# Optimization experiments

Hardware: AMD Instinct MI355X
Metric: run time of the kernel (lower is better)

Reference implementation:

```python
import jax, jax.numpy as jnp
import numpy as np

B, M, H, E, V, U = 1024, 15, 256, 256, 30000, 1000


def setup_inputs() -> dict:
    key = jax.random.key(0)
    ks = jax.random.split(key, 24)
    s = 0.05  # weight init scale
    return {
        "input_ids": jax.random.randint(ks[0], (B, 1), 0, V),
        "input_embedding": jax.random.normal(ks[1], (B, 1, E), jnp.float32),
        "hidden": jax.random.normal(ks[2], (1, B, H), jnp.float32),
        "inter_output": jax.random.normal(ks[3], (B, M, H), jnp.float32),
        "user_list": jax.random.randint(ks[4], (B,), 0, U),
        # per-user parameter tables (torch ModuleLists of Linear); stored [in,out]
        "inter_W": jax.random.normal(ks[5], (U, H, H), jnp.float32) * s,
        "inter_b": jax.random.normal(ks[6], (U, H), jnp.float32) * s,
        "hidden_W": jax.random.normal(ks[7], (U, H, H), jnp.float32) * s,
        "hidden_b": jax.random.normal(ks[8], (U, H), jnp.float32) * s,
        "lt1_W": jax.random.normal(ks[9], (U, 2 * H, H), jnp.float32) * s,
        "lt1_b": jax.random.normal(ks[10], (U, H), jnp.float32) * s,
        "scale_W": jax.random.normal(ks[11], (U, H), jnp.float32) * s,
        "scale_b": jax.random.normal(ks[12], (U,), jnp.float32) * s,
        # GRU (1 layer), torch layout: W_ih [3H, 2E], W_hh [3H, H], gate order r,z,n
        "gru_Wih": jax.random.normal(ks[13], (3 * H, 2 * E), jnp.float32) * s,
        "gru_Whh": jax.random.normal(ks[14], (3 * H, H), jnp.float32) * s,
        "gru_bih": jax.random.normal(ks[15], (3 * H,), jnp.float32) * s,
        "gru_bhh": jax.random.normal(ks[16], (3 * H,), jnp.float32) * s,
        # output projection, stored [H, V]
        "lin_W": jax.random.normal(ks[17], (H, V), jnp.float32) * s,
        "lin_b": jax.random.normal(ks[18], (V,), jnp.float32) * s,
    }


def reference(input_ids, input_embedding, hidden, inter_output, user_list,
              inter_W, inter_b, hidden_W, hidden_b, lt1_W, lt1_b,
              scale_W, scale_b, gru_Wih, gru_Whh, gru_bih, gru_bhh,
              lin_W, lin_b):
    embedded_input = input_embedding  # dropout p=0 (eval)
    hidden_t = jnp.transpose(hidden, (1, 0, 2))  # [B,1,H]

    # per-user intra attention: gather user weights, batched GEMMs (replaces python loop)
    Wi = inter_W[user_list]                      # [B,H,H]
    inter_output_a = jnp.einsum('bmh,bho->bmo', inter_output, Wi) + inter_b[user_list][:, None, :]
    Wh = hidden_W[user_list]                     # [B,H,H]
    hidden_t_a = jnp.einsum('bih,bho->bio', hidden_t, Wh) + hidden_b[user_list][:, None, :]  # [B,1,H]
    cat = jnp.concatenate([jnp.broadcast_to(hidden_t_a, (hidden_t_a.shape[0], M, H)), inter_output_a], axis=2)  # [B,M,2H]
    result = jnp.tanh(jnp.einsum('bmk,bko->bmo', cat, lt1_W[user_list]) + lt1_b[user_list][:, None, :])  # [B,M,H]
    energies = jnp.einsum('bmh,bh->bm', result, scale_W[user_list]) + scale_b[user_list][:, None]  # [B,M]

    attn_weights = jax.nn.softmax(energies, axis=1)                      # [B,M]
    context = jnp.einsum('bm,bmh->bh', attn_weights, inter_output)[:, None, :]  # [B,1,H]

    gru_input = jnp.concatenate([embedded_input, context], axis=2)  # [B,1,2E]
    x = gru_input[:, 0, :]
    h = hidden[0]
    gi = x @ gru_Wih.T + gru_bih   # [B,3H]
    gh = h @ gru_Whh.T + gru_bhh
    gi_r, gi_z, gi_n = jnp.split(gi, 3, axis=1)
    gh_r, gh_z, gh_n = jnp.split(gh, 3, axis=1)
    r = jax.nn.sigmoid(gi_r + gh_r)
    z = jax.nn.sigmoid(gi_z + gh_z)
    n = jnp.tanh(gi_n + r * gh_n)
    h_new = (1.0 - z) * n + z * h
    gru_output = h_new[:, None, :]       # [B,1,H]
    hidden_new = h_new[None, :, :]       # [1,B,H]

    output = gru_output @ lin_W + lin_b  # [B,1,V]
    return (output, hidden_new, embedded_input, gru_output, attn_weights)
```

## Files before the change

kernel.cpp:

```cpp
#include <hip/hip_runtime.h>
#include <math.h>

#define B 1024
#define M 15
#define H 256
#define E 256
#define V 30000
#define U 1000

typedef float  vf4    __attribute__((ext_vector_type(4)));
typedef __bf16 bf16x8 __attribute__((ext_vector_type(8)));
typedef float  f32x4  __attribute__((ext_vector_type(4)));

#define O_OUT   0
#define O_HID   ((size_t)B*V)
#define O_EMB   (O_HID + (size_t)B*H)
#define O_GRU   (O_EMB + (size_t)B*E)
#define O_ATT   (O_GRU + (size_t)B*H)

#define GLDS(g, l) __builtin_amdgcn_global_load_lds( \
    (const __attribute__((address_space(1))) void*)(g), \
    (__attribute__((address_space(3))) void*)(l), 16, 0, 0)

union BF8 { __bf16 h[8]; bf16x8 v; };
union BF4 { __bf16 h[4]; unsigned long long u; };

__global__ __launch_bounds__(1024) void sort_kernel(
    const int* __restrict__ ul, int* __restrict__ order, int* __restrict__ rbase_g)
{
    __shared__ int cnt[1024];
    __shared__ int base[1024];
    const int tid = threadIdx.x;
    cnt[tid] = 0;
    __syncthreads();
    const int u = ul[tid];
    atomicAdd(&cnt[u], 1);
    __syncthreads();
    int c0 = cnt[tid];
    int v  = c0;
    for (int off = 1; off < 1024; off <<= 1) {
        int add = (tid >= off) ? cnt[tid - off] : 0;
        __syncthreads();
        v += add;
        cnt[tid] = v;
        __syncthreads();
    }
    base[tid]   = v - c0;
    rbase_g[tid] = v - c0;
    __syncthreads();
    int pos = atomicAdd(&base[u], 1);
    order[pos] = tid;
}

#define FB_ATTN 1024
#define FB_TR   500
#define FB_WC   256
#define FB_TOT  (FB_ATTN + FB_TR + FB_WC)

__global__ __launch_bounds__(256, 3) void fused_pre_kernel(
    const float* __restrict__ hidden,
    const float* __restrict__ inter_output,
    const int*   __restrict__ user_list,
    const int*   __restrict__ order,
    const int*   __restrict__ rbase,
    const float* __restrict__ inter_W,
    const float* __restrict__ inter_b,
    const float* __restrict__ hidden_W,
    const float* __restrict__ hidden_b,
    const float* __restrict__ lt1_W,
    const float* __restrict__ lt1_b,
    const float* __restrict__ scale_W,
    const float* __restrict__ scale_b,
    const float* __restrict__ emb,
    const float* __restrict__ Wih,
    const float* __restrict__ Whh,
    const float* __restrict__ lin_W,
    float* __restrict__ out,
    __bf16* __restrict__ xcat,
    __bf16* __restrict__ wcat,
    __bf16* __restrict__ WT)
{
    __shared__ __align__(16) char smem[34432];
    const int bid = blockIdx.x;
    const int tid = threadIdx.x;

    if (bid >= FB_ATTN + FB_TR) {
        const int wb   = bid - (FB_ATTN + FB_TR);
        const int wave = tid >> 6, lane = tid & 63;
        const int n    = wb * 4 + wave;
        const int r    = (n >> 2) + ((n & 3) << 8);
        #pragma unroll
        for (int i = 0; i < 3; ++i) {
            int k = i * 256 + lane * 4;
            vf4 v = {0.f, 0.f, 0.f, 0.f};
            if (r < 512) {
                v = (k < 512) ? *(const vf4*)&Wih[(size_t)r * 512 + k]
                              : *(const vf4*)&Whh[(size_t)r * 256 + (k - 512)];
            } else if (r < 768) {
                if (k < 512) v = *(const vf4*)&Wih[(size_t)r * 512 + k];
            } else {
                if (k >= 512) v = *(const vf4*)&Whh[(size_t)(r - 256) * 256 + (k - 512)];
            }
            BF4 p;
            p.h[0]=(__bf16)v[0]; p.h[1]=(__bf16)v[1]; p.h[2]=(__bf16)v[2]; p.h[3]=(__bf16)v[3];
            *(unsigned long long*)&wcat[(size_t)n * 768 + k] = p.u;
        }
        return;
    }

    if (bid >= FB_ATTN) {
        const int t   = bid - FB_ATTN;
        const int v0  = (t % 125) * 240;
        const int k0  = (t / 125) * 64;
        const int lane = tid & 63, kq = tid >> 6;
        __bf16* T = (__bf16*)smem;

        if (lane < 60) {
            #pragma unroll
            for (int i = 0; i < 4; ++i) {
                int kr = kq * 16 + i * 4;
                vf4 f0 = *(const vf4*)&lin_W[(size_t)(k0 + kr + 0) * V + v0 + lane * 4];
                vf4 f1 = *(const vf4*)&lin_W[(size_t)(k0 + kr + 1) * V + v0 + lane * 4];
                vf4 f2 = *(const vf4*)&lin_W[(size_t)(k0 + kr + 2) * V + v0 + lane * 4];
                vf4 f3 = *(const vf4*)&lin_W[(size_t)(k0 + kr + 3) * V + v0 + lane * 4];
                #pragma unroll
                for (int j = 0; j < 4; ++j) {
                    BF4 pk;
                    pk.h[0] = (__bf16)f0[j];
                    pk.h[1] = (__bf16)f1[j];
                    pk.h[2] = (__bf16)f2[j];
                    pk.h[3] = (__bf16)f3[j];
                    int v = lane * 4 + j;
                    *(unsigned long long*)&T[v * 68 + kr] = pk.u;
                }
            }
        }
        __syncthreads();
        for (int r = 0; r < 15; ++r) {
            int L = r * 256 + tid;
            int v = L >> 4, c = L & 15;
            __builtin_nontemporal_store(
                *(const unsigned long long*)&T[v * 68 + c * 4],
                (unsigned long long*)&WT[(size_t)(v0 + v) * H + k0 + c * 4]);
        }
        return;
    }

    const int s   = ((bid & 7) << 7) + (bid >> 3);
    const int b0  = order[s];
    const int u   = user_list[b0];

    {
        float ev = emb[(size_t)b0 * E + tid];
        float hv = hidden[(size_t)b0 * H + tid];
        xcat[(size_t)b0 * 768 + tid]       = (__bf16)ev;
        xcat[(size_t)b0 * 768 + 512 + tid] = (__bf16)hv;
        __builtin_nontemporal_store(ev, &out[O_EMB + (size_t)b0 * E + tid]);
    }

    if ((s - rbase[u]) & 1) return;
    bool paired = false;
    int  b1 = b0;
    if (s + 1 < B) {
        int ob = order[s + 1];
        if (user_list[ob] == u) { paired = true; b1 = ob; }
    }

    const int lane = tid & 63;
    const int wave = tid >> 6;
    const int wn0  = wave * 64;

    __bf16* Abuf = (__bf16*)smem;
    __bf16* hta  = (__bf16*)(smem + 32768);
    float*  red  = (float*)(smem + 32768 + 1024);
    float*  e_lds= (float*)(smem + 32768 + 1024 + 512);

    {
        const int r    = tid >> 3;
        const int part = tid & 7;
        const int sm   = r >> 4;
        const int mr   = r & 15;
        const int bs   = sm ? b1 : b0;
        const bool zr  = (sm == 1) && !paired;
        #pragma unroll
        for (int it = 0; it < 8; ++it) {
            int c = part + it * 8;
            int k = c * 8;
            BF8 p;
            #pragma unroll
            for (int j = 0; j < 8; ++j) p.h[j] = (__bf16)0.f;
            if (!zr) {
                if (mr < 15 && k < 256) {
                    vf4 f0 = *(const vf4*)&inter_output[(size_t)bs * M * H + mr * H + k];
                    vf4 f1 = *(const vf4*)&inter_output[(size_t)bs * M * H + mr * H + k + 4];
                    p.h[0]=(__bf16)f0[0]; p.h[1]=(__bf16)f0[1]; p.h[2]=(__bf16)f0[2]; p.h[3]=(__bf16)f0[3];
                    p.h[4]=(__bf16)f1[0]; p.h[5]=(__bf16)f1[1]; p.h[6]=(__bf16)f1[2]; p.h[7]=(__bf16)f1[3];
                } else if (mr == 15 && k >= 256) {
                    vf4 f0 = *(const vf4*)&hidden[(size_t)bs * H + (k - 256)];
                    vf4 f1 = *(const vf4*)&hidden[(size_t)bs * H + (k - 256) + 4];
                    p.h[0]=(__bf16)f0[0]; p.h[1]=(__bf16)f0[1]; p.h[2]=(__bf16)f0[2]; p.h[3]=(__bf16)f0[3];
                    p.h[4]=(__bf16)f1[0]; p.h[5]=(__bf16)f1[1]; p.h[6]=(__bf16)f1[2]; p.h[7]=(__bf16)f1[3];
                }
            }
            *(bf16x8*)&Abuf[r * 512 + (c ^ (r & 7)) * 8] = p.v;
        }
    }
    __syncthreads();

    const float* Wi_base  = inter_W  + (size_t)u * H * H;
    const float* Wh_base  = hidden_W + (size_t)u * H * H;
    const float* lt1_base = lt1_W    + (size_t)u * 2 * H * H;

    const int ocol = wn0 + (lane & 15);
    const int krow = (lane >> 4) * 8;

    f32x4 acc1[2][4];
    #pragma unroll
    for (int mf = 0; mf < 2; ++mf)
        #pragma unroll
        for (int nf = 0; nf < 4; ++nf) { f32x4 z = {0.f,0.f,0.f,0.f}; acc1[mf][nf] = z; }

    #pragma unroll 2
    for (int ks = 0; ks < 16; ++ks) {
        const float* Bp = ((ks < 8) ? (Wi_base + (size_t)(ks * 32) * H)
                                    : (Wh_base + (size_t)((ks - 8) * 32) * H))
                          + (size_t)krow * H + ocol;
        float t[4][8];
        #pragma unroll
        for (int j = 0; j < 8; ++j)
            #pragma unroll
            for (int nf = 0; nf < 4; ++nf)
                t[nf][j] = Bp[(size_t)j * H + nf * 16];
        bf16x8 bfr[4];
        #pragma unroll
        for (int nf = 0; nf < 4; ++nf) {
            BF8 pk;
            #pragma unroll
            for (int j = 0; j < 8; ++j) pk.h[j] = (__bf16)t[nf][j];
            bfr[nf] = pk.v;
        }
        int sca = ((ks * 4 + (lane >> 4)) ^ (lane & 7)) * 8;
        bf16x8 a0 = *(const bf16x8*)&Abuf[(lane & 15) * 512 + sca];
        #pragma unroll
        for (int nf = 0; nf < 4; ++nf)
            acc1[0][nf] = __builtin_amdgcn_mfma_f32_16x16x32_bf16(a0, bfr[nf], acc1[0][nf], 0, 0, 0);
        if (paired) {
            bf16x8 a1 = *(const bf16x8*)&Abuf[(16 + (lane & 15)) * 512 + sca];
            #pragma unroll
            for (int nf = 0; nf < 4; ++nf)
                acc1[1][nf] = __builtin_amdgcn_mfma_f32_16x16x32_bf16(a1, bfr[nf], acc1[1][nf], 0, 0, 0);
        }
    }
    __syncthreads();

    if ((lane >> 4) == 3) {
        #pragma unroll
        for (int nf = 0; nf < 4; ++nf) {
            int o = wn0 + nf * 16 + (lane & 15);
            float hb = hidden_b[(size_t)u * H + o];
            hta[o]       = (__bf16)(acc1[0][nf][3] + hb);
            hta[256 + o] = (__bf16)(acc1[1][nf][3] + hb);
        }
    }
    #pragma unroll
    for (int mf = 0; mf < 2; ++mf) {
        #pragma unroll
        for (int nf = 0; nf < 4; ++nf) {
            int o  = wn0 + nf * 16 + (lane & 15);
            float bi = inter_b[(size_t)u * H + o];
            int k  = 256 + o;
            #pragma unroll
            for (int j = 0; j < 4; ++j) {
                int r  = mf * 16 + (lane >> 4) * 4 + j;
                Abuf[r * 512 + ((k >> 3) ^ (r & 7)) * 8 + (k & 7)] = (__bf16)(acc1[mf][nf][j] + bi);
            }
        }
    }
    __syncthreads();

    {
        const int r    = tid >> 3;
        const int part = tid & 7;
        const int sm   = r >> 4;
        #pragma unroll
        for (int it = 0; it < 4; ++it) {
            int c = part + it * 8;
            bf16x8 hv = *(const bf16x8*)&hta[sm * 256 + c * 8];
            *(bf16x8*)&Abuf[r * 512 + (c ^ (r & 7)) * 8] = hv;
        }
    }
    __syncthreads();

    f32x4 acc2[2][4];
    #pragma unroll
    for (int mf = 0; mf < 2; ++mf)
        #pragma unroll
        for (int nf = 0; nf < 4; ++nf) { f32x4 z = {0.f,0.f,0.f,0.f}; acc2[mf][nf] = z; }

    #pragma unroll 2
    for (int ks = 0; ks < 16; ++ks) {
        const float* Bp = lt1_base + (size_t)(ks * 32) * H + (size_t)krow * H + ocol;
        float t[4][8];
        #pragma unroll
        for (int j = 0; j < 8; ++j)
            #pragma unroll
            for (int nf = 0; nf < 4; ++nf)
                t[nf][j] = Bp[(size_t)j * H + nf * 16];
        bf16x8 bfr[4];
        #pragma unroll
        for (int nf = 0; nf < 4; ++nf) {
            BF8 pk;
            #pragma unroll
            for (int j = 0; j < 8; ++j) pk.h[j] = (__bf16)t[nf][j];
            bfr[nf] = pk.v;
        }
        int sca = ((ks * 4 + (lane >> 4)) ^ (lane & 7)) * 8;
        bf16x8 a0 = *(const bf16x8*)&Abuf[(lane & 15) * 512 + sca];
        #pragma unroll
        for (int nf = 0; nf < 4; ++nf)
            acc2[0][nf] = __builtin_amdgcn_mfma_f32_16x16x32_bf16(a0, bfr[nf], acc2[0][nf], 0, 0, 0);
        if (paired) {
            bf16x8 a1 = *(const bf16x8*)&Abuf[(16 + (lane & 15)) * 512 + sca];
            #pragma unroll
            for (int nf = 0; nf < 4; ++nf)
                acc2[1][nf] = __builtin_amdgcn_mfma_f32_16x16x32_bf16(a1, bfr[nf], acc2[1][nf], 0, 0, 0);
        }
    }

    float p0[4] = {0.f,0.f,0.f,0.f};
    float p1[4] = {0.f,0.f,0.f,0.f};
    #pragma unroll
    for (int nf = 0; nf < 4; ++nf) {
        int o = wn0 + nf * 16 + (lane & 15);
        float l1b = lt1_b[(size_t)u * H + o];
        float sw  = scale_W[(size_t)u * H + o];
        #pragma unroll
        for (int j = 0; j < 4; ++j)
            p0[j] += tanhf(acc2[0][nf][j] + l1b) * sw;
        if (paired)
            #pragma unroll
            for (int j = 0; j < 4; ++j)
                p1[j] += tanhf(acc2[1][nf][j] + l1b) * sw;
    }
    #pragma unroll
    for (int j = 0; j < 4; ++j) {
        float v = p0[j];
        v += __shfl_xor(v, 1, 64); v += __shfl_xor(v, 2, 64);
        v += __shfl_xor(v, 4, 64); v += __shfl_xor(v, 8, 64);
        if ((lane & 15) == 0) red[0 * 64 + wave * 16 + (lane >> 4) * 4 + j] = v;
        float w = p1[j];
        w += __shfl_xor(w, 1, 64); w += __shfl_xor(w, 2, 64);
        w += __shfl_xor(w, 4, 64); w += __shfl_xor(w, 8, 64);
        if ((lane & 15) == 0) red[1 * 64 + wave * 16 + (lane >> 4) * 4 + j] = w;
    }
    __syncthreads();
    if (tid < 32) {
        int sm = tid >> 4, mm = tid & 15;
        e_lds[sm * 16 + mm] = red[sm * 64 + mm] + red[sm * 64 + 16 + mm]
                            + red[sm * 64 + 32 + mm] + red[sm * 64 + 48 + mm]
                            + scale_b[u];
    }
    __syncthreads();

    const int nsm = paired ? 2 : 1;
    for (int sm = 0; sm < nsm; ++sm) {
        const int bs = sm ? b1 : b0;
        float mx = -1e30f;
        #pragma unroll
        for (int m = 0; m < M; ++m) mx = fmaxf(mx, e_lds[sm * 16 + m]);
        float sum = 0.f;
        float aw[M];
        #pragma unroll
        for (int m = 0; m < M; ++m) { aw[m] = expf(e_lds[sm * 16 + m] - mx); sum += aw[m]; }
        float inv = 1.f / sum;
        if (tid < M)
            __builtin_nontemporal_store(aw[tid] * inv, &out[O_ATT + (size_t)bs * M + tid]);
        float ctx = 0.f;
        #pragma unroll
        for (int m = 0; m < M; ++m)
            ctx += aw[m] * inter_output[(size_t)bs * M * H + m * H + tid];
        xcat[(size_t)bs * 768 + 256 + tid] = (__bf16)(ctx * inv);
    }
}

__global__ __launch_bounds__(256) void xgemm_gate_kernel(
    const __bf16* __restrict__ xcat, const __bf16* __restrict__ wcat,
    const float* __restrict__ hidden,
    const float* __restrict__ bih, const float* __restrict__ bhh,
    float* __restrict__ out, __bf16* __restrict__ hnb)
{
    const int n0   = blockIdx.x * 64;
    const int m0   = blockIdx.y * 64;
    const int tid  = threadIdx.x;
    const int wave = tid >> 6, lane = tid & 63;
    const int wm   = wave >> 1, wn = wave & 1;

    __shared__ __align__(16) __bf16 Al[64 * 128];
    __shared__ __align__(16) __bf16 Bl[64 * 128];
    __shared__ __align__(16) float  Cs[64 * 68];

    f32x4 acc[2][2];
    #pragma unroll
    for (int mf = 0; mf < 2; ++mf)
        #pragma unroll
        for (int nf = 0; nf < 2; ++nf) { f32x4 z = {0.f,0.f,0.f,0.f}; acc[mf][nf] = z; }

    for (int ks = 0; ks < 6; ++ks) {
        #pragma unroll
        for (int r = 0; r < 4; ++r) {
            int L = r * 256 + tid;
            int row = L >> 4, c = L & 15;
            int sc = c ^ (row & 7);
            GLDS(xcat + (size_t)(m0 + row) * 768 + ks * 128 + sc * 8, &Al[(size_t)L * 8]);
        }
        #pragma unroll
        for (int r = 0; r < 4; ++r) {
            int L = r * 256 + tid;
            int row = L >> 4, c = L & 15;
            int sc = c ^ (row & 7);
            GLDS(wcat + (size_t)(n0 + row) * 768 + ks * 128 + sc * 8, &Bl[(size_t)L * 8]);
        }
        __syncthreads();
        #pragma unroll
        for (int kk = 0; kk < 4; ++kk) {
            bf16x8 af[2];
            #pragma unroll
            for (int mf = 0; mf < 2; ++mf) {
                int row = wm * 32 + mf * 16 + (lane & 15);
                int c   = kk * 4 + (lane >> 4);
                af[mf] = *(const bf16x8*)&Al[row * 128 + (c ^ (row & 7)) * 8];
            }
            bf16x8 bfr[2];
            #pragma unroll
            for (int nf = 0; nf < 2; ++nf) {
                int col = wn * 32 + nf * 16 + (lane & 15);
                int c   = kk * 4 + (lane >> 4);
                bfr[nf] = *(const bf16x8*)&Bl[col * 128 + (c ^ (col & 7)) * 8];
            }
            #pragma unroll
            for (int mf = 0; mf < 2; ++mf)
                #pragma unroll
                for (int nf = 0; nf < 2; ++nf)
                    acc[mf][nf] = __builtin_amdgcn_mfma_f32_16x16x32_bf16(
                        af[mf], bfr[nf], acc[mf][nf], 0, 0, 0);
        }
        __syncthreads();
    }

    #pragma unroll
    for (int nf = 0; nf < 2; ++nf) {
        int lc = wn * 32 + nf * 16 + (lane & 15);
        #pragma unroll
        for (int mf = 0; mf < 2; ++mf) {
            int lr = wm * 32 + mf * 16 + (lane >> 4) * 4;
            f32x4 a = acc[mf][nf];
            #pragma unroll
            for (int j = 0; j < 4; ++j)
                Cs[(lr + j) * 68 + lc] = a[j];
        }
    }
    __syncthreads();

    #pragma unroll
    for (int k = 0; k < 4; ++k) {
        int idx = k * 256 + tid;
        int r = idx >> 4, g = idx & 15;
        f32x4 c = *(const f32x4*)&Cs[r * 68 + g * 4];
        int b = m0 + r;
        int j = (n0 >> 2) + g;
        float rs  = c[0] + bih[j]       + bhh[j];
        float zs  = c[1] + bih[256 + j] + bhh[256 + j];
        float gin = c[2] + bih[512 + j];
        float ghn = c[3] + bhh[512 + j];
        float h   = hidden[(size_t)b * H + j];
        float r_  = 1.f / (1.f + expf(-rs));
        float z_  = 1.f / (1.f + expf(-zs));
        float n_  = tanhf(gin + r_ * ghn);
        float hn  = (1.f - z_) * n_ + z_ * h;
        __builtin_nontemporal_store(hn, &out[O_HID + (size_t)b * H + j]);
        __builtin_nontemporal_store(hn, &out[O_GRU + (size_t)b * H + j]);
        hnb[(size_t)b * H + j] = (__bf16)hn;
    }
}

#define GBM 64
#define GBN 128
#define GBK 64
#define NTM 16
#define NTN 235
#define NWG (NTN * NTM)
__global__ __launch_bounds__(256, 3) void out_mfma_kernel(
    const __bf16* __restrict__ hnb,
    const __bf16* __restrict__ WT,
    const float* __restrict__ lin_b,
    float* __restrict__ out)
{
    const int L  = blockIdx.x;
    const int s  = (L & 7) * (NWG / 8) + (L >> 3);
    const int nt = s >> 4, mt = s & 15;
    const int n0 = nt * GBN;
    const int m0 = mt * GBM;
    const int tid  = threadIdx.x;
    const int wave = tid >> 6, lane = tid & 63;

    __shared__ __align__(16) char gsm[GBM * H * 2 + GBN * GBK * 2];
    __bf16* Al = (__bf16*)gsm;
    __bf16* Bl = (__bf16*)(gsm + GBM * H * 2);

    #pragma unroll
    for (int r = 0; r < 8; ++r) {
        int Li = r * 256 + tid;
        int m = Li >> 5;
        int c = Li & 31;
        int sc = c ^ (m & 7);
        GLDS(hnb + (size_t)(m0 + m) * H + sc * 8, &Al[(size_t)Li * 8]);
    }

    f32x4 acc[4][2];
    #pragma unroll
    for (int mf = 0; mf < 4; ++mf)
        #pragma unroll
        for (int nf = 0; nf < 2; ++nf) {
            f32x4 z = {0.f, 0.f, 0.f, 0.f};
            acc[mf][nf] = z;
        }

    const int wn0 = wave * 32;

    for (int ks = 0; ks < 4; ++ks) {
        #pragma unroll
        for (int r = 0; r < 4; ++r) {
            int Li = r * 256 + tid;
            int n = Li >> 3;
            int c = Li & 7;
            int sc = c ^ (n & 7);
            int nn = n0 + n; if (nn >= V) nn = V - 1;
            GLDS(WT + (size_t)nn * H + ks * GBK + sc * 8, &Bl[(size_t)Li * 8]);
        }
        __syncthreads();

        #pragma unroll
        for (int kk = 0; kk < 2; ++kk) {
            bf16x8 af[4];
            #pragma unroll
            for (int mf = 0; mf < 4; ++mf) {
                int row = mf * 16 + (lane & 15);
                int c   = ks * 8 + kk * 4 + (lane >> 4);
                int cs  = c ^ (row & 7);
                af[mf] = *(const bf16x8*)&Al[row * H + cs * 8];
            }
            bf16x8 bfr[2];
            #pragma unroll
            for (int nf = 0; nf < 2; ++nf) {
                int col = wn0 + nf * 16 + (lane & 15);
                int c   = kk * 4 + (lane >> 4);
                int cs  = c ^ (col & 7);
                bfr[nf] = *(const bf16x8*)&Bl[col * GBK + cs * 8];
            }
            #pragma unroll
            for (int mf = 0; mf < 4; ++mf)
                #pragma unroll
                for (int nf = 0; nf < 2; ++nf)
                    acc[mf][nf] = __builtin_amdgcn_mfma_f32_16x16x32_bf16(
                        af[mf], bfr[nf], acc[mf][nf], 0, 0, 0);
        }
        __syncthreads();
    }

    float* Cs = (float*)gsm;
    #pragma unroll
    for (int nf = 0; nf < 2; ++nf) {
        int col = wn0 + nf * 16 + (lane & 15);
        #pragma unroll
        for (int mf = 0; mf < 4; ++mf) {
            #pragma unroll
            for (int j = 0; j < 4; ++j)
                Cs[(mf * 16 + (lane >> 4) * 4 + j) * 128 + col] = acc[mf][nf][j];
        }
    }
    __syncthreads();

    const int c4 = tid & 31;
    const bool nok = (n0 + c4 * 4 + 3 < V);
    f32x4 lb = {0.f, 0.f, 0.f, 0.f};
    if (nok) lb = *(const f32x4*)&lin_b[n0 + c4 * 4];
    #pragma unroll
    for (int it = 0; it < 8; ++it) {
        int idx = it * 256 + tid;
        int r = idx >> 5;
        f32x4 c = *(const f32x4*)&Cs[r * 128 + c4 * 4];
        c += lb;
        if (nok)
            __builtin_nontemporal_store(c, (f32x4*)&out[(size_t)(m0 + r) * V + n0 + c4 * 4]);
    }
}

extern "C" void kernel_launch(void* const* d_in, const int* in_sizes, int n_in,
                              void* d_out, int out_size, void* d_ws, size_t ws_size,
                              hipStream_t stream) {
    const float* emb    = (const float*)d_in[1];
    const float* hidden = (const float*)d_in[2];
    const float* io     = (const float*)d_in[3];
    const int*   ul     = (const int*)  d_in[4];
    const float* iW     = (const float*)d_in[5];
    const float* ib     = (const float*)d_in[6];
    const float* hW     = (const float*)d_in[7];
    const float* hb     = (const float*)d_in[8];
    const float* l1W    = (const float*)d_in[9];
    const float* l1b    = (const float*)d_in[10];
    const float* sW     = (const float*)d_in[11];
    const float* sb     = (const float*)d_in[12];
    const float* Wih    = (const float*)d_in[13];
    const float* Whh    = (const float*)d_in[14];
    const float* bih    = (const float*)d_in[15];
    const float* bhh    = (const float*)d_in[16];
    const float* lW     = (const float*)d_in[17];
    const float* lb     = (const float*)d_in[18];

    float* out = (float*)d_out;
    char* ws = (char*)d_ws;
    int*    order = (int*)ws;
    int*    rbase = (int*)(ws + 4096);
    __bf16* xcat  = (__bf16*)(ws + 8192);
    __bf16* wcat  = (__bf16*)(ws + 8192 + 1572864);
    __bf16* hnb   = (__bf16*)(ws + 8192 + 2 * 1572864);
    __bf16* WT    = (__bf16*)(ws + 8192 + 2 * 1572864 + 524288);

    sort_kernel<<<1, 1024, 0, stream>>>(ul, order, rbase);
    fused_pre_kernel<<<FB_TOT, 256, 0, stream>>>(
        hidden, io, ul, order, rbase, iW, ib, hW, hb, l1W, l1b, sW, sb,
        emb, Wih, Whh, lW, out, xcat, wcat, WT);
    xgemm_gate_kernel<<<dim3(16, 16), 256, 0, stream>>>(xcat, wcat, hidden, bih, bhh, out, hnb);
    out_mfma_kernel<<<NWG, 256, 0, stream>>>(hnb, WT, lb, out);
}
```

Measured before the change: 232.5 us.

## Move weight conversion into the sort kernel and split attention into its own kernel

The single-block sort kernel now also runs the lin_W transpose/bf16 conversion and the GRU weight packing, using 1024-thread blocks. Before, that kernel used one workgroup while the rest of the GPU sat idle, and the conversion blocks were mixed into the heavy attention kernel. The attention part becomes a separate kernel with only the per-batch work. This fills the otherwise idle sort launch and simplifies the attention kernel. The price is larger 1024-thread blocks with different occupancy for the conversion, and conversion and attention can no longer overlap inside one launch.

```diff
diff --git a/kernel.cpp b/kernel.cpp
--- a/kernel.cpp
+++ b/kernel.cpp
@@ -25,39 +25,110 @@
 union BF8 { __bf16 h[8]; bf16x8 v; };
 union BF4 { __bf16 h[4]; unsigned long long u; };
 
-__global__ __launch_bounds__(1024) void sort_kernel(
-    const int* __restrict__ ul, int* __restrict__ order, int* __restrict__ rbase_g)
+#define K1_TR   500
+#define K1_WC   64
+#define K1_TOT  (1 + K1_TR + K1_WC)
+
+__global__ __launch_bounds__(1024) void pre_kernel(
+    const int*   __restrict__ ul,
+    const float* __restrict__ Wih,
+    const float* __restrict__ Whh,
+    const float* __restrict__ lin_W,
+    int* __restrict__ order, int* __restrict__ rbase_g,
+    __bf16* __restrict__ wcat,
+    __bf16* __restrict__ WT)
 {
-    __shared__ int cnt[1024];
-    __shared__ int base[1024];
+    __shared__ __align__(16) char smem[32640];
+    const int bid = blockIdx.x;
     const int tid = threadIdx.x;
-    cnt[tid] = 0;
-    __syncthreads();
-    const int u = ul[tid];
-    atomicAdd(&cnt[u], 1);
-    __syncthreads();
-    int c0 = cnt[tid];
-    int v  = c0;
-    for (int off = 1; off < 1024; off <<= 1) {
-        int add = (tid >= off) ? cnt[tid - off] : 0;
-        __syncthreads();
-        v += add;
-        cnt[tid] = v;
-        __syncthreads();
-    }
-    base[tid]   = v - c0;
-    rbase_g[tid] = v - c0;
-    __syncthreads();
-    int pos = atomicAdd(&base[u], 1);
-    order[pos] = tid;
+
+    if (bid == 0) {
+        __shared__ int cnt[1024];
+        __shared__ int base[1024];
+        cnt[tid] = 0;
+        __syncthreads();
+        const int u = ul[tid];
+        atomicAdd(&cnt[u], 1);
+        __syncthreads();
+        int c0 = cnt[tid];
+        int v  = c0;
+        for (int off = 1; off < 1024; off <<= 1) {
+            int add = (tid >= off) ? cnt[tid - off] : 0;
+            __syncthreads();
+            v += add;
+            cnt[tid] = v;
+            __syncthreads();
+        }
+        base[tid]    = v - c0;
+        rbase_g[tid] = v - c0;
+        __syncthreads();
+        int pos = atomicAdd(&base[u], 1);
+        order[pos] = tid;
+        return;
+    }
+
+    if (bid <= K1_TR) {
+        const int t   = bid - 1;
+        const int v0  = (t % 125) * 240;
+        const int k0  = (t / 125) * 64;
+        const int lane = tid & 63, kq = tid >> 6;
+        __bf16* T = (__bf16*)smem;
+
+        if (lane < 60) {
+            int kr = kq * 4;
+            vf4 f0 = *(const vf4*)&lin_W[(size_t)(k0 + kr + 0) * V + v0 + lane * 4];
+            vf4 f1 = *(const vf4*)&lin_W[(size_t)(k0 + kr + 1) * V + v0 + lane * 4];
+            vf4 f2 = *(const vf4*)&lin_W[(size_t)(k0 + kr + 2) * V + v0 + lane * 4];
+            vf4 f3 = *(const vf4*)&lin_W[(size_t)(k0 + kr + 3) * V + v0 + lane * 4];
+            #pragma unroll
+            for (int j = 0; j < 4; ++j) {
+                BF4 pk;
+                pk.h[0] = (__bf16)f0[j];
+                pk.h[1] = (__bf16)f1[j];
+                pk.h[2] = (__bf16)f2[j];
+                pk.h[3] = (__bf16)f3[j];
+                int v = lane * 4 + j;
+                *(unsigned long long*)&T[v * 68 + kr] = pk.u;
+            }
+        }
+        __syncthreads();
+        #pragma unroll
+        for (int r = 0; r < 4; ++r) {
+            int L = r * 1024 + tid;
+            int v = L >> 4, c = L & 15;
+            if (v < 240)
+                __builtin_nontemporal_store(
+                    *(const unsigned long long*)&T[v * 68 + c * 4],
+                    (unsigned long long*)&WT[(size_t)(v0 + v) * H + k0 + c * 4]);
+        }
+        return;
+    }
+
+    {
+        const int wb   = bid - 1 - K1_TR;
+        const int lane = tid & 63;
+        const int n    = wb * 16 + (tid >> 6);
+        const int r    = (n >> 2) + ((n & 3) << 8);
+        #pragma unroll
+        for (int i = 0; i < 3; ++i) {
+            int k = i * 256 + lane * 4;
+            vf4 v = {0.f, 0.f, 0.f, 0.f};
+            if (r < 512) {
+                v = (k < 512) ? *(const vf4*)&Wih[(size_t)r * 512 + k]
+                              : *(const vf4*)&Whh[(size_t)r * 256 + (k - 512)];
+            } else if (r < 768) {
+                if (k < 512) v = *(const vf4*)&Wih[(size_t)r * 512 + k];
+            } else {
+                if (k >= 512) v = *(const vf4*)&Whh[(size_t)(r - 256) * 256 + (k - 512)];
+            }
+            BF4 p;
+            p.h[0]=(__bf16)v[0]; p.h[1]=(__bf16)v[1]; p.h[2]=(__bf16)v[2]; p.h[3]=(__bf16)v[3];
+            *(unsigned long long*)&wcat[(size_t)n * 768 + k] = p.u;
+        }
+    }
 }
 
-#define FB_ATTN 1024
-#define FB_TR   500
-#define FB_WC   256
-#define FB_TOT  (FB_ATTN + FB_TR + FB_WC)
-
-__global__ __launch_bounds__(256, 3) void fused_pre_kernel(
+__global__ __launch_bounds__(256, 3) void attn_kernel(
     const float* __restrict__ hidden,
     const float* __restrict__ inter_output,
     const int*   __restrict__ user_list,
@@ -72,79 +143,12 @@
     const float* __restrict__ scale_W,
     const float* __restrict__ scale_b,
     const float* __restrict__ emb,
-    const float* __restrict__ Wih,
-    const float* __restrict__ Whh,
-    const float* __restrict__ lin_W,
     float* __restrict__ out,
-    __bf16* __restrict__ xcat,
-    __bf16* __restrict__ wcat,
-    __bf16* __restrict__ WT)
+    __bf16* __restrict__ xcat)
 {
     __shared__ __align__(16) char smem[34432];
     const int bid = blockIdx.x;
     const int tid = threadIdx.x;
-
-    if (bid >= FB_ATTN + FB_TR) {
-        const int wb   = bid - (FB_ATTN + FB_TR);
-        const int wave = tid >> 6, lane = tid & 63;
-        const int n    = wb * 4 + wave;
-        const int r    = (n >> 2) + ((n & 3) << 8);
-        #pragma unroll
-        for (int i = 0; i < 3; ++i) {
-            int k = i * 256 + lane * 4;
-            vf4 v = {0.f, 0.f, 0.f, 0.f};
-            if (r < 512) {
-                v = (k < 512) ? *(const vf4*)&Wih[(size_t)r * 512 + k]
-                              : *(const vf4*)&Whh[(size_t)r * 256 + (k - 512)];
-            } else if (r < 768) {
-                if (k < 512) v = *(const vf4*)&Wih[(size_t)r * 512 + k];
-            } else {
-                if (k >= 512) v = *(const vf4*)&Whh[(size_t)(r - 256) * 256 + (k - 512)];
-            }
-            BF4 p;
-            p.h[0]=(__bf16)v[0]; p.h[1]=(__bf16)v[1]; p.h[2]=(__bf16)v[2]; p.h[3]=(__bf16)v[3];
-            *(unsigned long long*)&wcat[(size_t)n * 768 + k] = p.u;
-        }
-        return;
-    }
-
-    if (bid >= FB_ATTN) {
-        const int t   = bid - FB_ATTN;
-        const int v0  = (t % 125) * 240;
-        const int k0  = (t / 125) * 64;
-        const int lane = tid & 63, kq = tid >> 6;
-        __bf16* T = (__bf16*)smem;
-
-        if (lane < 60) {
-            #pragma unroll
-            for (int i = 0; i < 4; ++i) {
-                int kr = kq * 16 + i * 4;
-                vf4 f0 = *(const vf4*)&lin_W[(size_t)(k0 + kr + 0) * V + v0 + lane * 4];
-                vf4 f1 = *(const vf4*)&lin_W[(size_t)(k0 + kr + 1) * V + v0 + lane * 4];
-                vf4 f2 = *(const vf4*)&lin_W[(size_t)(k0 + kr + 2) * V + v0 + lane * 4];
-                vf4 f3 = *(const vf4*)&lin_W[(size_t)(k0 + kr + 3) * V + v0 + lane * 4];
-                #pragma unroll
-                for (int j = 0; j < 4; ++j) {
-                    BF4 pk;
-                    pk.h[0] = (__bf16)f0[j];
-                    pk.h[1] = (__bf16)f1[j];
-                    pk.h[2] = (__bf16)f2[j];
-                    pk.h[3] = (__bf16)f3[j];
-                    int v = lane * 4 + j;
-                    *(unsigned long long*)&T[v * 68 + kr] = pk.u;
-                }
-            }
-        }
-        __syncthreads();
-        for (int r = 0; r < 15; ++r) {
-            int L = r * 256 + tid;
-            int v = L >> 4, c = L & 15;
-            __builtin_nontemporal_store(
-                *(const unsigned long long*)&T[v * 68 + c * 4],
-                (unsigned long long*)&WT[(size_t)(v0 + v) * H + k0 + c * 4]);
-        }
-        return;
-    }
 
     const int s   = ((bid & 7) << 7) + (bid >> 3);
     const int b0  = order[s];
@@ -626,10 +630,9 @@
     __bf16* hnb   = (__bf16*)(ws + 8192 + 2 * 1572864);
     __bf16* WT    = (__bf16*)(ws + 8192 + 2 * 1572864 + 524288);
 
-    sort_kernel<<<1, 1024, 0, stream>>>(ul, order, rbase);
-    fused_pre_kernel<<<FB_TOT, 256, 0, stream>>>(
-        hidden, io, ul, order, rbase, iW, ib, hW, hb, l1W, l1b, sW, sb,
-        emb, Wih, Whh, lW, out, xcat, wcat, WT);
+    pre_kernel<<<K1_TOT, 1024, 0, stream>>>(ul, Wih, Whh, lW, order, rbase, wcat, WT);
+    attn_kernel<<<B, 256, 0, stream>>>(hidden, io, ul, order, rbase, iW, ib, hW, hb,
+                                       l1W, l1b, sW, sb, emb, out, xcat);
     xgemm_gate_kernel<<<dim3(16, 16), 256, 0, stream>>>(xcat, wcat, hidden, bih, bhh, out, hnb);
     out_mfma_kernel<<<NWG, 256, 0, stream>>>(hnb, WT, lb, out);
 }
```

Measured after the change: 224.5 us, median of 2. 1.04x faster.
